# Kernel optimization log

Hardware: AMD Instinct MI355X
Metric: run time of the kernel (lower is better)

## Reference

```python
import jax, jax.numpy as jnp
import numpy as np

SCALE = 0.1
TEMP = 1.0
LN_EPS = 1e-6
NORM_EPS = 1e-12  # torch F.normalize eps


def setup_inputs() -> dict:
    key = jax.random.key(0)
    k1, = jax.random.split(key, 1)
    B, N, D = 8, 2048, 256
    x = jax.random.normal(k1, (B, N, D), dtype=jnp.float32)
    ln_gamma = jnp.ones((D,), dtype=jnp.float32)
    ln_beta = jnp.zeros((D,), dtype=jnp.float32)
    return {"x": x, "ln_gamma": ln_gamma, "ln_beta": ln_beta}


def reference(x, ln_gamma, ln_beta):
    # L2-normalize along feature dim (torch F.normalize, dim=2)
    norm = jnp.sqrt(jnp.sum(x * x, axis=2, keepdims=True))
    xn = x / jnp.maximum(norm, NORM_EPS)
    # self-similarity: [B, N, N]
    sim = jnp.einsum('bnd,bmd->bnm', xn, xn) / TEMP
    # dual_norm: row softmax + column softmax
    sim = jax.nn.softmax(sim, axis=2) + jax.nn.softmax(sim, axis=1)
    x_neg = jnp.einsum('bnm,bmd->bnd', sim, x)
    x = x - SCALE * x_neg
    # LayerNorm(dim), eps=1e-6
    mu = jnp.mean(x, axis=-1, keepdims=True)
    var = jnp.mean((x - mu) ** 2, axis=-1, keepdims=True)
    xhat = (x - mu) * jax.lax.rsqrt(var + LN_EPS)
    return xhat * ln_gamma + ln_beta
```

## Files before the change

kernel.cpp:

```cpp
#include <hip/hip_runtime.h>

namespace {
constexpr int Bv = 8;
constexpr int Nv = 2048;
constexpr int Dv = 256;
constexpr float SCALE = 0.1f;
constexpr float PSCALE = 256.0f;
constexpr float OSC = SCALE / PSCALE;
constexpr float LN_EPS = 1e-6f;
constexpr float NORM_EPS = 1e-12f;
}

typedef unsigned char u8;
typedef unsigned int u32;
typedef __attribute__((ext_vector_type(4))) float f32x4;

__device__ __forceinline__ void gll16(const void* g, void* l) {
    __builtin_amdgcn_global_load_lds(
        (__attribute__((address_space(1))) void*)(uintptr_t)g,
        (__attribute__((address_space(3))) void*)(uintptr_t)l, 16, 0, 0);
}
__device__ __forceinline__ u32 pk4(float a, float b, float c, float d) {
    u32 w = __builtin_amdgcn_cvt_pk_fp8_f32(a, b, 0, false);
    return __builtin_amdgcn_cvt_pk_fp8_f32(c, d, w, true);
}

__global__ __launch_bounds__(512) void k_prepT(const float* __restrict__ x,
                                               u8* __restrict__ xn8,
                                               u8* __restrict__ xTf) {
    __shared__ u8 lt[64][272];
    const int b = blockIdx.x >> 5;
    const int n0 = (blockIdx.x & 31) * 64;
    const int t = threadIdx.x;
    const int r = t >> 3, c0 = (t & 7) * 32;
    const float* xr = x + ((size_t)b * Nv + n0 + r) * Dv + c0;
    float4 v[8];
    float ss = 0.f;
#pragma unroll
    for (int i = 0; i < 8; ++i) {
        v[i] = ((const float4*)xr)[i];
        ss += v[i].x * v[i].x + v[i].y * v[i].y + v[i].z * v[i].z + v[i].w * v[i].w;
    }
#pragma unroll
    for (int m = 1; m < 8; m <<= 1) ss += __shfl_xor(ss, m, 64);
    const float inv = 1.0f / fmaxf(sqrtf(ss), NORM_EPS);
    u32 wn[8];
#pragma unroll
    for (int i = 0; i < 8; ++i) {
        wn[i] = pk4(v[i].x * inv, v[i].y * inv, v[i].z * inv, v[i].w * inv);
        *(u32*)&lt[r][c0 + i * 4] = pk4(v[i].x, v[i].y, v[i].z, v[i].w);
    }
    {
        uint4 o0 = {wn[0], wn[1], wn[2], wn[3]};
        uint4 o1 = {wn[4], wn[5], wn[6], wn[7]};
        u8* xnr = xn8 + ((size_t)b * Nv + n0 + r) * Dv + c0;
        *(uint4*)xnr = o0;
        *(uint4*)(xnr + 16) = o1;
    }
    __syncthreads();
    {
        u8* xtb = xTf + (size_t)b * 524288;
        const int d = t >> 1, h = t & 1;
        const int g = d >> 4, l = d & 15;
#pragma unroll
        for (int q = 0; q < 4; ++q) {
            const int nb = h * 32 + q * 8;
            u32 lo = (u32)lt[nb][d] | ((u32)lt[nb + 1][d] << 8) |
                     ((u32)lt[nb + 2][d] << 16) | ((u32)lt[nb + 3][d] << 24);
            u32 hi = (u32)lt[nb + 4][d] | ((u32)lt[nb + 5][d] << 8) |
                     ((u32)lt[nb + 6][d] << 16) | ((u32)lt[nb + 7][d] << 24);
            uint2 o = {lo, hi};
            const int c = (n0 >> 3) + h * 4 + q;
            *(uint2*)&xtb[g * 32768 + c * 128 + l * 8] = o;
        }
    }
}

__global__ __launch_bounds__(512, 4) void k_gemm1(const u8* __restrict__ xn8,
                                                  u8* __restrict__ E,
                                                  float* __restrict__ lsum) {
    __shared__ u8 Bs[2][128 * 256];
    __shared__ u8 eS[2][128 * 40];
    __shared__ float red[32][4];
    const int wg = blockIdx.x;
    const int b = wg & 7, bi = wg >> 3;
    const int t = threadIdx.x;
    const int wave = t >> 6, lane = t & 63;
    const int wr = wave >> 2, wc = wave & 3;
    const int l15 = lane & 15, kl = lane >> 4;
    const u8* xb = xn8 + (size_t)b * (Nv * Dv);

    auto stageB = [&](int buf, int ch) {
#pragma unroll
        for (int c = 0; c < 4; ++c) {
            const int row = wave * 16 + c * 4 + (lane >> 4);
            const int slot = (lane & 15) ^ (row & 15);
            gll16(xb + (size_t)(ch * 128 + row) * Dv + slot * 16,
                  Bs[buf] + wave * 4096 + c * 1024);
        }
    };
    auto bfrag = [&](const u8* base, int row, int kk) -> long {
        const int slot = kk * 2 + (kl >> 1);
        return *(const long*)(base + row * 256 +
                              ((slot ^ (row & 15)) << 4) + ((kl & 1) << 3));
    };

    const int ch0 = bi >> 2;
    stageB(0, ch0);
    __syncthreads();
    long af[8];
    {
        const int arow = (bi & 3) * 32 + wr * 16 + l15;
#pragma unroll
        for (int kk = 0; kk < 8; ++kk) af[kk] = bfrag(Bs[0], arow, kk);
    }
    float rs[4] = {0.f, 0.f, 0.f, 0.f};
    u8* Eb = E + (size_t)b * Nv * Nv;
    int cur = 0;
    for (int cc = 0; cc < 16; ++cc) {
        const int ch = (ch0 + cc) & 15;
        if (cc < 15) stageB(cur ^ 1, (ch0 + cc + 1) & 15);
        f32x4 acc[2] = {};
#pragma unroll
        for (int kk = 0; kk < 8; ++kk) {
            const long b0 = bfrag(Bs[cur], wc * 32 + l15, kk);
            const long b1 = bfrag(Bs[cur], wc * 32 + 16 + l15, kk);
            acc[0] = __builtin_amdgcn_mfma_f32_16x16x32_fp8_fp8(af[kk], b0, acc[0], 0, 0, 0);
            acc[1] = __builtin_amdgcn_mfma_f32_16x16x32_fp8_fp8(af[kk], b1, acc[1], 0, 0, 0);
        }
#pragma unroll
        for (int j = 0; j < 2; ++j) {
            const int col = wc * 32 + j * 16 + l15;
            const float e0 = __expf(acc[j][0] - 1.0f);
            const float e1 = __expf(acc[j][1] - 1.0f);
            const float e2 = __expf(acc[j][2] - 1.0f);
            const float e3 = __expf(acc[j][3] - 1.0f);
            rs[0] += e0; rs[1] += e1; rs[2] += e2; rs[3] += e3;
            *(u32*)&eS[cur][col * 40 + wr * 16 + kl * 4] = pk4(e0, e1, e2, e3);
        }
        __syncthreads();
        {
            const int c = t >> 2, sg = t & 3;
            *(uint2*)&Eb[(size_t)(ch * 128 + c) * Nv + bi * 32 + sg * 8] =
                *(const uint2*)&eS[cur][c * 40 + sg * 8];
        }
        cur ^= 1;
    }
#pragma unroll
    for (int r = 0; r < 4; ++r) {
        float v = rs[r];
#pragma unroll
        for (int m = 1; m < 16; m <<= 1) v += __shfl_xor(v, m, 64);
        if (l15 == 0) red[wr * 16 + kl * 4 + r][wc] = v;
    }
    __syncthreads();
    if (t < 32)
        lsum[b * Nv + bi * 32 + t] = red[t][0] + red[t][1] + red[t][2] + red[t][3];
}

__global__ __launch_bounds__(512) void k_gemm2ln(const u8* __restrict__ E,
                                                 const float* __restrict__ lsum,
                                                 const u8* __restrict__ xTf,
                                                 const float* __restrict__ x,
                                                 const float* __restrict__ gamma,
                                                 const float* __restrict__ beta,
                                                 float* __restrict__ out) {
    __shared__ u8 Ps[2][32 * 152];
    __shared__ float rlv[Nv];
    __shared__ float red[32][4][2];
    const int wg = blockIdx.x;
    const int swz = (wg & 7) * 64 + (wg >> 3);
    const int b = swz >> 6, bi = swz & 63;
    const int t = threadIdx.x;
    const int wave = t >> 6, lane = t & 63;
    const int wr = wave >> 2, wc = wave & 3;
    const int l15 = lane & 15, kl = lane >> 4;
    const int srow = t >> 4, s16 = t & 15;
    const float* lsb = lsum + (size_t)b * Nv;
    const u8* Erow = E + ((size_t)b * Nv + bi * 32 + srow) * Nv + s16 * 8;
    const u8* xtb = xTf + (size_t)b * 524288;
    float linv_n;

#pragma unroll
    for (int q = 0; q < 4; ++q) {
        const int m = q * 512 + t;
        rlv[m] = PSCALE * __builtin_amdgcn_rcpf(lsb[m]);
    }
    const u8* bB[4];
#pragma unroll
    for (int j = 0; j < 4; ++j)
        bB[j] = xtb + (wc * 4 + j) * 32768 + kl * 128 + l15 * 8;

    auto wstore = [&](u8* pbuf, uint2 ev, int k0) {
        const float* rp = &rlv[k0 + s16 * 8];
        const float4 r0 = *(const float4*)(rp);
        const float4 r1 = *(const float4*)(rp + 4);
        const u32 o0 = pk4(__builtin_amdgcn_cvt_f32_fp8(ev.x, 0) * (linv_n + r0.x),
                           __builtin_amdgcn_cvt_f32_fp8(ev.x, 1) * (linv_n + r0.y),
                           __builtin_amdgcn_cvt_f32_fp8(ev.x, 2) * (linv_n + r0.z),
                           __builtin_amdgcn_cvt_f32_fp8(ev.x, 3) * (linv_n + r0.w));
        const u32 o1 = pk4(__builtin_amdgcn_cvt_f32_fp8(ev.y, 0) * (linv_n + r1.x),
                           __builtin_amdgcn_cvt_f32_fp8(ev.y, 1) * (linv_n + r1.y),
                           __builtin_amdgcn_cvt_f32_fp8(ev.y, 2) * (linv_n + r1.z),
                           __builtin_amdgcn_cvt_f32_fp8(ev.y, 3) * (linv_n + r1.w));
        uint2 o = {o0, o1};
        *(uint2*)(pbuf + srow * 152 + s16 * 8) = o;
    };

    uint2 evB = *(const uint2*)(Erow);
    __syncthreads();
    linv_n = rlv[bi * 32 + srow];
    wstore(Ps[0], evB, 0);
    evB = *(const uint2*)(Erow + 128);
    uint2 evC = *(const uint2*)(Erow + 256);
    __syncthreads();

    const int aoff = (wr * 16 + l15) * 152 + kl * 8;
    f32x4 acc[4] = {};
    int cur = 0;
    for (int kt = 0; kt < 16; ++kt) {
        const u8* pc = Ps[cur];
#pragma unroll
        for (int kk = 0; kk < 4; ++kk) {
            const long a0 = *(const long*)(pc + aoff + kk * 32);
            const long b0 = *(const long*)(bB[0] + kt * 2048 + kk * 512);
            const long b1 = *(const long*)(bB[1] + kt * 2048 + kk * 512);
            const long b2 = *(const long*)(bB[2] + kt * 2048 + kk * 512);
            const long b3 = *(const long*)(bB[3] + kt * 2048 + kk * 512);
            acc[0] = __builtin_amdgcn_mfma_f32_16x16x32_fp8_fp8(a0, b0, acc[0], 0, 0, 0);
            acc[1] = __builtin_amdgcn_mfma_f32_16x16x32_fp8_fp8(a0, b1, acc[1], 0, 0, 0);
            acc[2] = __builtin_amdgcn_mfma_f32_16x16x32_fp8_fp8(a0, b2, acc[2], 0, 0, 0);
            acc[3] = __builtin_amdgcn_mfma_f32_16x16x32_fp8_fp8(a0, b3, acc[3], 0, 0, 0);
        }
        if (kt < 15) {
            wstore(Ps[cur ^ 1], evB, (kt + 1) * 128);
            evB = evC;
            if (kt < 14) evC = *(const uint2*)(Erow + (kt + 2) * 128);
        }
        __syncthreads();
        cur ^= 1;
    }
    const float* xb = x + ((size_t)b * Nv + bi * 32) * Dv;
    float tv[4][4];
#pragma unroll
    for (int r = 0; r < 4; ++r) {
        const int rr = wr * 16 + kl * 4 + r;
        float s1 = 0.f, s2 = 0.f;
#pragma unroll
        for (int j = 0; j < 4; ++j) {
            const int cc = wc * 64 + j * 16 + l15;
            const float v = xb[(size_t)rr * Dv + cc] - OSC * acc[j][r];
            tv[j][r] = v;
            s1 += v; s2 += v * v;
        }
#pragma unroll
        for (int m = 1; m < 16; m <<= 1) {
            s1 += __shfl_xor(s1, m, 64);
            s2 += __shfl_xor(s2, m, 64);
        }
        if (l15 == 0) { red[rr][wc][0] = s1; red[rr][wc][1] = s2; }
    }
    __syncthreads();
#pragma unroll
    for (int r = 0; r < 4; ++r) {
        const int rr = wr * 16 + kl * 4 + r;
        const float s1 = red[rr][0][0] + red[rr][1][0] + red[rr][2][0] + red[rr][3][0];
        const float s2 = red[rr][0][1] + red[rr][1][1] + red[rr][2][1] + red[rr][3][1];
        const float mu = s1 * (1.0f / Dv);
        const float var = s2 * (1.0f / Dv) - mu * mu;
        const float rstd = rsqrtf(var + LN_EPS);
#pragma unroll
        for (int j = 0; j < 4; ++j) {
            const int cc = wc * 64 + j * 16 + l15;
            out[((size_t)b * Nv + bi * 32 + rr) * Dv + cc] =
                (tv[j][r] - mu) * rstd * gamma[cc] + beta[cc];
        }
    }
}

extern "C" void kernel_launch(void* const* d_in, const int* in_sizes, int n_in,
                              void* d_out, int out_size, void* d_ws, size_t ws_size,
                              hipStream_t stream) {
    const float* x = (const float*)d_in[0];
    const float* gamma = (const float*)d_in[1];
    const float* beta = (const float*)d_in[2];
    float* out = (float*)d_out;
    char* ws = (char*)d_ws;
    u8* xn8 = (u8*)ws;
    u8* xTf = (u8*)(ws + 4194304);
    float* lsum = (float*)(ws + 8388608);
    u8* E = (u8*)(ws + 8454144);

    k_prepT<<<Bv * (Nv / 64), 512, 0, stream>>>(x, xn8, xTf);
    k_gemm1<<<Bv * (Nv / 32), 512, 0, stream>>>(xn8, E, lsum);
    k_gemm2ln<<<Bv * (Nv / 32), 512, 0, stream>>>(E, lsum, xTf, x, gamma, beta, out);
}
```

Baseline: 77.90 us.

## Stage transposed fp8 B operand through LDS with async loads in gemm2

Changes the transposed fp8 x layout to a plain row-major [D][N] array. In the second GEMM, that operand is now staged into double-buffered LDS with global_load_lds using an XOR swizzle, instead of each wave reading MFMA fragments straight from global memory. The wave tiling becomes 32x32 per wave, and the reciprocal row sums are computed once in gemm1 and streamed per K tile rather than preloaded into LDS. This adds 64KB of LDS per block, which may lower occupancy, in exchange for coalesced, overlapped B loads.

```diff
diff --git a/kernel.cpp b/kernel.cpp
--- a/kernel.cpp
+++ b/kernel.cpp
@@ -27,7 +27,7 @@
 
 __global__ __launch_bounds__(512) void k_prepT(const float* __restrict__ x,
                                                u8* __restrict__ xn8,
-                                               u8* __restrict__ xTf) {
+                                               u8* __restrict__ xT8) {
     __shared__ u8 lt[64][272];
     const int b = blockIdx.x >> 5;
     const int n0 = (blockIdx.x & 31) * 64;
@@ -59,26 +59,25 @@
     }
     __syncthreads();
     {
-        u8* xtb = xTf + (size_t)b * 524288;
         const int d = t >> 1, h = t & 1;
-        const int g = d >> 4, l = d & 15;
-#pragma unroll
-        for (int q = 0; q < 4; ++q) {
-            const int nb = h * 32 + q * 8;
-            u32 lo = (u32)lt[nb][d] | ((u32)lt[nb + 1][d] << 8) |
-                     ((u32)lt[nb + 2][d] << 16) | ((u32)lt[nb + 3][d] << 24);
-            u32 hi = (u32)lt[nb + 4][d] | ((u32)lt[nb + 5][d] << 8) |
-                     ((u32)lt[nb + 6][d] << 16) | ((u32)lt[nb + 7][d] << 24);
-            uint2 o = {lo, hi};
-            const int c = (n0 >> 3) + h * 4 + q;
-            *(uint2*)&xtb[g * 32768 + c * 128 + l * 8] = o;
-        }
+        u32 w2[8];
+#pragma unroll
+        for (int q = 0; q < 8; ++q) {
+            const int nb = h * 32 + q * 4;
+            w2[q] = (u32)lt[nb][d] | ((u32)lt[nb + 1][d] << 8) |
+                    ((u32)lt[nb + 2][d] << 16) | ((u32)lt[nb + 3][d] << 24);
+        }
+        uint4 p0 = {w2[0], w2[1], w2[2], w2[3]};
+        uint4 p1 = {w2[4], w2[5], w2[6], w2[7]};
+        u8* xtr = xT8 + ((size_t)b * Dv + d) * Nv + n0 + h * 32;
+        *(uint4*)xtr = p0;
+        *(uint4*)(xtr + 16) = p1;
     }
 }
 
 __global__ __launch_bounds__(512, 4) void k_gemm1(const u8* __restrict__ xn8,
                                                   u8* __restrict__ E,
-                                                  float* __restrict__ lsum) {
+                                                  float* __restrict__ rl) {
     __shared__ u8 Bs[2][128 * 256];
     __shared__ u8 eS[2][128 * 40];
     __shared__ float red[32][4];
@@ -155,125 +154,141 @@
     }
     __syncthreads();
     if (t < 32)
-        lsum[b * Nv + bi * 32 + t] = red[t][0] + red[t][1] + red[t][2] + red[t][3];
+        rl[b * Nv + bi * 32 + t] =
+            PSCALE * __builtin_amdgcn_rcpf(red[t][0] + red[t][1] + red[t][2] + red[t][3]);
 }
 
 __global__ __launch_bounds__(512) void k_gemm2ln(const u8* __restrict__ E,
-                                                 const float* __restrict__ lsum,
-                                                 const u8* __restrict__ xTf,
+                                                 const float* __restrict__ rl,
+                                                 const u8* __restrict__ xT8,
                                                  const float* __restrict__ x,
                                                  const float* __restrict__ gamma,
                                                  const float* __restrict__ beta,
                                                  float* __restrict__ out) {
-    __shared__ u8 Ps[2][32 * 152];
-    __shared__ float rlv[Nv];
-    __shared__ float red[32][4][2];
+    __shared__ u8 Bs[2][256 * 128];
+    __shared__ u8 Ps[2][32 * 136];
+    __shared__ float red[32][8][2];
     const int wg = blockIdx.x;
     const int swz = (wg & 7) * 64 + (wg >> 3);
     const int b = swz >> 6, bi = swz & 63;
     const int t = threadIdx.x;
     const int wave = t >> 6, lane = t & 63;
-    const int wr = wave >> 2, wc = wave & 3;
     const int l15 = lane & 15, kl = lane >> 4;
     const int srow = t >> 4, s16 = t & 15;
-    const float* lsb = lsum + (size_t)b * Nv;
+    const float* rlb = rl + (size_t)b * Nv;
     const u8* Erow = E + ((size_t)b * Nv + bi * 32 + srow) * Nv + s16 * 8;
-    const u8* xtb = xTf + (size_t)b * 524288;
-    float linv_n;
-
-#pragma unroll
-    for (int q = 0; q < 4; ++q) {
-        const int m = q * 512 + t;
-        rlv[m] = PSCALE * __builtin_amdgcn_rcpf(lsb[m]);
-    }
-    const u8* bB[4];
-#pragma unroll
-    for (int j = 0; j < 4; ++j)
-        bB[j] = xtb + (wc * 4 + j) * 32768 + kl * 128 + l15 * 8;
-
-    auto wstore = [&](u8* pbuf, uint2 ev, int k0) {
-        const float* rp = &rlv[k0 + s16 * 8];
-        const float4 r0 = *(const float4*)(rp);
-        const float4 r1 = *(const float4*)(rp + 4);
-        const u32 o0 = pk4(__builtin_amdgcn_cvt_f32_fp8(ev.x, 0) * (linv_n + r0.x),
-                           __builtin_amdgcn_cvt_f32_fp8(ev.x, 1) * (linv_n + r0.y),
-                           __builtin_amdgcn_cvt_f32_fp8(ev.x, 2) * (linv_n + r0.z),
-                           __builtin_amdgcn_cvt_f32_fp8(ev.x, 3) * (linv_n + r0.w));
-        const u32 o1 = pk4(__builtin_amdgcn_cvt_f32_fp8(ev.y, 0) * (linv_n + r1.x),
-                           __builtin_amdgcn_cvt_f32_fp8(ev.y, 1) * (linv_n + r1.y),
-                           __builtin_amdgcn_cvt_f32_fp8(ev.y, 2) * (linv_n + r1.z),
-                           __builtin_amdgcn_cvt_f32_fp8(ev.y, 3) * (linv_n + r1.w));
+    const u8* xtb = xT8 + (size_t)b * 524288;
+
+    auto issueB = [&](int buf, int kt) {
+#pragma unroll
+        for (int c = 0; c < 4; ++c) {
+            const int row = c * 64 + wave * 8 + (lane >> 3);
+            const int slot = (lane & 7) ^ (row & 7);
+            gll16(xtb + (size_t)row * Nv + kt * 128 + slot * 16,
+                  (char*)Bs[buf] + c * 8192 + wave * 1024);
+        }
+    };
+    auto bfragB = [&](const u8* base, int d, int kk) -> long {
+        const int s = kk * 2 + (kl >> 1);
+        return *(const long*)(base + d * 128 + ((s ^ (d & 7)) << 4) + ((kl & 1) << 3));
+    };
+    auto afrag = [&](const u8* base, int row, int kk) -> long {
+        return *(const long*)(base + row * 136 + kk * 32 + kl * 8);
+    };
+
+    const float linv_n = rlb[bi * 32 + srow];
+    auto wstore = [&](u8* pbuf, uint2 ev, float4 ra, float4 rb) {
+        const u32 o0 = pk4(__builtin_amdgcn_cvt_f32_fp8(ev.x, 0) * (linv_n + ra.x),
+                           __builtin_amdgcn_cvt_f32_fp8(ev.x, 1) * (linv_n + ra.y),
+                           __builtin_amdgcn_cvt_f32_fp8(ev.x, 2) * (linv_n + ra.z),
+                           __builtin_amdgcn_cvt_f32_fp8(ev.x, 3) * (linv_n + ra.w));
+        const u32 o1 = pk4(__builtin_amdgcn_cvt_f32_fp8(ev.y, 0) * (linv_n + rb.x),
+                           __builtin_amdgcn_cvt_f32_fp8(ev.y, 1) * (linv_n + rb.y),
+                           __builtin_amdgcn_cvt_f32_fp8(ev.y, 2) * (linv_n + rb.z),
+                           __builtin_amdgcn_cvt_f32_fp8(ev.y, 3) * (linv_n + rb.w));
         uint2 o = {o0, o1};
-        *(uint2*)(pbuf + srow * 152 + s16 * 8) = o;
-    };
-
+        *(uint2*)(pbuf + srow * 136 + s16 * 8) = o;
+    };
+
+    issueB(0, 0);
     uint2 evB = *(const uint2*)(Erow);
-    __syncthreads();
-    linv_n = rlv[bi * 32 + srow];
-    wstore(Ps[0], evB, 0);
+    float4 raB = *(const float4*)&rlb[s16 * 8];
+    float4 rbB = *(const float4*)&rlb[s16 * 8 + 4];
+    wstore(Ps[0], evB, raB, rbB);
     evB = *(const uint2*)(Erow + 128);
     uint2 evC = *(const uint2*)(Erow + 256);
-    __syncthreads();
-
-    const int aoff = (wr * 16 + l15) * 152 + kl * 8;
-    f32x4 acc[4] = {};
+    raB = *(const float4*)&rlb[128 + s16 * 8];
+    rbB = *(const float4*)&rlb[128 + s16 * 8 + 4];
+    __syncthreads();
+
+    f32x4 acc[2][2] = {};
     int cur = 0;
     for (int kt = 0; kt < 16; ++kt) {
-        const u8* pc = Ps[cur];
+        if (kt < 15) issueB(cur ^ 1, kt + 1);
 #pragma unroll
         for (int kk = 0; kk < 4; ++kk) {
-            const long a0 = *(const long*)(pc + aoff + kk * 32);
-            const long b0 = *(const long*)(bB[0] + kt * 2048 + kk * 512);
-            const long b1 = *(const long*)(bB[1] + kt * 2048 + kk * 512);
-            const long b2 = *(const long*)(bB[2] + kt * 2048 + kk * 512);
-            const long b3 = *(const long*)(bB[3] + kt * 2048 + kk * 512);
-            acc[0] = __builtin_amdgcn_mfma_f32_16x16x32_fp8_fp8(a0, b0, acc[0], 0, 0, 0);
-            acc[1] = __builtin_amdgcn_mfma_f32_16x16x32_fp8_fp8(a0, b1, acc[1], 0, 0, 0);
-            acc[2] = __builtin_amdgcn_mfma_f32_16x16x32_fp8_fp8(a0, b2, acc[2], 0, 0, 0);
-            acc[3] = __builtin_amdgcn_mfma_f32_16x16x32_fp8_fp8(a0, b3, acc[3], 0, 0, 0);
+            const long a0 = afrag(Ps[cur], l15, kk);
+            const long a1 = afrag(Ps[cur], 16 + l15, kk);
+            const long b0 = bfragB(Bs[cur], wave * 32 + l15, kk);
+            const long b1 = bfragB(Bs[cur], wave * 32 + 16 + l15, kk);
+            acc[0][0] = __builtin_amdgcn_mfma_f32_16x16x32_fp8_fp8(a0, b0, acc[0][0], 0, 0, 0);
+            acc[0][1] = __builtin_amdgcn_mfma_f32_16x16x32_fp8_fp8(a0, b1, acc[0][1], 0, 0, 0);
+            acc[1][0] = __builtin_amdgcn_mfma_f32_16x16x32_fp8_fp8(a1, b0, acc[1][0], 0, 0, 0);
+            acc[1][1] = __builtin_amdgcn_mfma_f32_16x16x32_fp8_fp8(a1, b1, acc[1][1], 0, 0, 0);
         }
         if (kt < 15) {
-            wstore(Ps[cur ^ 1], evB, (kt + 1) * 128);
+            wstore(Ps[cur ^ 1], evB, raB, rbB);
             evB = evC;
-            if (kt < 14) evC = *(const uint2*)(Erow + (kt + 2) * 128);
+            if (kt < 14) {
+                evC = *(const uint2*)(Erow + (kt + 2) * 128);
+                raB = *(const float4*)&rlb[(kt + 1) * 128 + s16 * 8];
+                rbB = *(const float4*)&rlb[(kt + 1) * 128 + s16 * 8 + 4];
+            }
         }
         __syncthreads();
         cur ^= 1;
     }
     const float* xb = x + ((size_t)b * Nv + bi * 32) * Dv;
-    float tv[4][4];
-#pragma unroll
-    for (int r = 0; r < 4; ++r) {
-        const int rr = wr * 16 + kl * 4 + r;
-        float s1 = 0.f, s2 = 0.f;
-#pragma unroll
-        for (int j = 0; j < 4; ++j) {
-            const int cc = wc * 64 + j * 16 + l15;
-            const float v = xb[(size_t)rr * Dv + cc] - OSC * acc[j][r];
-            tv[j][r] = v;
-            s1 += v; s2 += v * v;
-        }
-#pragma unroll
-        for (int m = 1; m < 16; m <<= 1) {
-            s1 += __shfl_xor(s1, m, 64);
-            s2 += __shfl_xor(s2, m, 64);
-        }
-        if (l15 == 0) { red[rr][wc][0] = s1; red[rr][wc][1] = s2; }
-    }
-    __syncthreads();
-#pragma unroll
-    for (int r = 0; r < 4; ++r) {
-        const int rr = wr * 16 + kl * 4 + r;
-        const float s1 = red[rr][0][0] + red[rr][1][0] + red[rr][2][0] + red[rr][3][0];
-        const float s2 = red[rr][0][1] + red[rr][1][1] + red[rr][2][1] + red[rr][3][1];
-        const float mu = s1 * (1.0f / Dv);
-        const float var = s2 * (1.0f / Dv) - mu * mu;
-        const float rstd = rsqrtf(var + LN_EPS);
-#pragma unroll
-        for (int j = 0; j < 4; ++j) {
-            const int cc = wc * 64 + j * 16 + l15;
-            out[((size_t)b * Nv + bi * 32 + rr) * Dv + cc] =
-                (tv[j][r] - mu) * rstd * gamma[cc] + beta[cc];
+    float tv[2][2][4];
+#pragma unroll
+    for (int i = 0; i < 2; ++i) {
+#pragma unroll
+        for (int r = 0; r < 4; ++r) {
+            const int rr = i * 16 + kl * 4 + r;
+            float s1 = 0.f, s2 = 0.f;
+#pragma unroll
+            for (int j = 0; j < 2; ++j) {
+                const int cc = wave * 32 + j * 16 + l15;
+                const float v = xb[(size_t)rr * Dv + cc] - OSC * acc[i][j][r];
+                tv[i][j][r] = v;
+                s1 += v; s2 += v * v;
+            }
+#pragma unroll
+            for (int m = 1; m < 16; m <<= 1) {
+                s1 += __shfl_xor(s1, m, 64);
+                s2 += __shfl_xor(s2, m, 64);
+            }
+            if (l15 == 0) { red[rr][wave][0] = s1; red[rr][wave][1] = s2; }
+        }
+    }
+    __syncthreads();
+#pragma unroll
+    for (int i = 0; i < 2; ++i) {
+#pragma unroll
+        for (int r = 0; r < 4; ++r) {
+            const int rr = i * 16 + kl * 4 + r;
+            float s1 = 0.f, s2 = 0.f;
+#pragma unroll
+            for (int w = 0; w < 8; ++w) { s1 += red[rr][w][0]; s2 += red[rr][w][1]; }
+            const float mu = s1 * (1.0f / Dv);
+            const float var = s2 * (1.0f / Dv) - mu * mu;
+            const float rstd = rsqrtf(var + LN_EPS);
+#pragma unroll
+            for (int j = 0; j < 2; ++j) {
+                const int cc = wave * 32 + j * 16 + l15;
+                out[((size_t)b * Nv + bi * 32 + rr) * Dv + cc] =
+                    (tv[i][j][r] - mu) * rstd * gamma[cc] + beta[cc];
+            }
         }
     }
 }
@@ -287,11 +302,11 @@
     float* out = (float*)d_out;
     char* ws = (char*)d_ws;
     u8* xn8 = (u8*)ws;
-    u8* xTf = (u8*)(ws + 4194304);
-    float* lsum = (float*)(ws + 8388608);
+    u8* xT8 = (u8*)(ws + 4194304);
+    float* rl = (float*)(ws + 8388608);
     u8* E = (u8*)(ws + 8454144);
 
-    k_prepT<<<Bv * (Nv / 64), 512, 0, stream>>>(x, xn8, xTf);
-    k_gemm1<<<Bv * (Nv / 32), 512, 0, stream>>>(xn8, E, lsum);
-    k_gemm2ln<<<Bv * (Nv / 32), 512, 0, stream>>>(E, lsum, xTf, x, gamma, beta, out);
-}
+    k_prepT<<<Bv * (Nv / 64), 512, 0, stream>>>(x, xn8, xT8);
+    k_gemm1<<<Bv * (Nv / 32), 512, 0, stream>>>(xn8, E, rl);
+    k_gemm2ln<<<Bv * (Nv / 32), 512, 0, stream>>>(E, rl, xT8, x, gamma, beta, out);
+}
```

Result: faster. 66.11 us, median of 2 (-15.1%).
